# Optimization experiments

Measured on AMD Instinct MI355X. Metric: run time of the kernel, lower is better.

The kernel has to match this reference:

```python
import jax, jax.numpy as jnp
import numpy as np

F = 1024      # features
CF = 768      # context_features
H = 8         # num_heads
D = 64        # head_features
MID = H * D   # 512
SCALE = D ** -0.5


def _ln(x, g, b):
    m = jnp.mean(x, axis=-1, keepdims=True)
    v = jnp.var(x, axis=-1, keepdims=True)
    return (x - m) / jnp.sqrt(v + 1e-5) * g + b


def _attention(x, ctx, ng, nb, ncg, ncb, wq, wkv, wo, bo):
    # pre-norms (Attention.forward)
    xn = _ln(x, ng, nb)
    cn = _ln(ctx, ncg, ncb)
    q = xn @ wq                              # [b, n, MID]
    k, v = jnp.split(cn @ wkv, 2, axis=-1)   # [b, m, MID] each
    b, n, _ = q.shape
    m = k.shape[1]
    q = q.reshape(b, n, H, D).transpose(0, 2, 1, 3)  # b h n d
    k = k.reshape(b, m, H, D).transpose(0, 2, 1, 3)
    v = v.reshape(b, m, H, D).transpose(0, 2, 1, 3)
    sim = jnp.einsum('bhnd,bhmd->bhnm', q, k) * SCALE   # use_rel_pos=False
    attn = jax.nn.softmax(sim, axis=-1)
    out = jnp.einsum('bhnm,bhmd->bhnd', attn, v)
    out = out.transpose(0, 2, 1, 3).reshape(b, n, MID)
    return out @ wo + bo


def setup_inputs() -> dict:
    key = jax.random.key(0)
    ks = jax.random.split(key, 16)
    s = 0.02
    inp = {
        'x': jax.random.normal(ks[0], (4, 2048, F), jnp.float32),
        'context': jax.random.normal(ks[1], (4, 512, CF), jnp.float32),
        # self-attention params
        'sa_ng': jnp.ones((F,), jnp.float32),
        'sa_nb': jnp.zeros((F,), jnp.float32),
        'sa_ncg': jnp.ones((F,), jnp.float32),
        'sa_ncb': jnp.zeros((F,), jnp.float32),
        'sa_wq': jax.random.normal(ks[2], (F, MID), jnp.float32) * s,
        'sa_wkv': jax.random.normal(ks[3], (F, 2 * MID), jnp.float32) * s,
        'sa_wo': jax.random.normal(ks[4], (MID, F), jnp.float32) * s,
        'sa_bo': jnp.zeros((F,), jnp.float32),
        # cross-attention params
        'ca_ng': jnp.ones((F,), jnp.float32),
        'ca_nb': jnp.zeros((F,), jnp.float32),
        'ca_ncg': jnp.ones((CF,), jnp.float32),
        'ca_ncb': jnp.zeros((CF,), jnp.float32),
        'ca_wq': jax.random.normal(ks[5], (F, MID), jnp.float32) * s,
        'ca_wkv': jax.random.normal(ks[6], (CF, 2 * MID), jnp.float32) * s,
        'ca_wo': jax.random.normal(ks[7], (MID, F), jnp.float32) * s,
        'ca_bo': jnp.zeros((F,), jnp.float32),
    }
    return inp


def reference(x, context,
              sa_ng, sa_nb, sa_ncg, sa_ncb, sa_wq, sa_wkv, sa_wo, sa_bo,
              ca_ng, ca_nb, ca_ncg, ca_ncb, ca_wq, ca_wkv, ca_wo, ca_bo):
    # AttentionBlock.forward: x = self_attn(x) + x; x = cross_attn(x, ctx) + x
    x = _attention(x, x, sa_ng, sa_nb, sa_ncg, sa_ncb, sa_wq, sa_wkv, sa_wo, sa_bo) + x
    x = _attention(x, context, ca_ng, ca_nb, ca_ncg, ca_ncb, ca_wq, ca_wkv, ca_wo, ca_bo) + x
    return x
```

## Files before the change

### kernel.cpp

```cpp
#include <hip/hip_runtime.h>
#include <hip/hip_bf16.h>

typedef __bf16 bf16x8 __attribute__((ext_vector_type(8)));
typedef float  f32x4  __attribute__((ext_vector_type(4)));

#define MFMA16(a, b, c) __builtin_amdgcn_mfma_f32_16x16x32_bf16((a), (b), (c), 0, 0, 0)

__device__ __forceinline__ float fast_exp2(float x) {
#if __has_builtin(__builtin_amdgcn_exp2f)
    return __builtin_amdgcn_exp2f(x);
#else
    return exp2f(x);
#endif
}

__device__ __forceinline__ void async16(void* lds, const void* g) {
    __builtin_amdgcn_global_load_lds(
        (const __attribute__((address_space(1))) unsigned int*)g,
        (__attribute__((address_space(3))) unsigned int*)lds, 16, 0, 0);
}

__device__ __forceinline__ unsigned cvt_pk_bf16(float lo, float hi) {
    unsigned r;
    asm("v_cvt_pk_bf16_f32 %0, %1, %2" : "=v"(r) : "v"(lo), "v"(hi));
    return r;
}
__device__ __forceinline__ void pl32(unsigned& a, unsigned& b) {
    asm volatile("v_permlane32_swap_b32 %0, %1" : "+v"(a), "+v"(b));
}
__device__ __forceinline__ void pl16(unsigned& a, unsigned& b) {
    asm volatile("v_permlane16_swap_b32 %0, %1" : "+v"(a), "+v"(b));
}

__device__ __forceinline__ void tconv_tile(const float* __restrict__ W,
                                           __bf16* __restrict__ WT,
                                           int K, int N, int id, int nbx,
                                           __bf16 (*t)[65]) {
    int n0 = (id % nbx) * 64, k0 = (id / nbx) * 64;
    int tx = threadIdx.x & 63, ty = threadIdx.x >> 6;
#pragma unroll
    for (int r = ty; r < 64; r += 4)
        t[r][tx] = (__bf16)W[(size_t)(k0 + r) * N + n0 + tx];
    __syncthreads();
#pragma unroll
    for (int rr = ty; rr < 64; rr += 4)
        WT[(size_t)(n0 + rr) * K + k0 + tx] = t[tx][rr];
}

__global__ __launch_bounds__(256) void tconv6_kernel(
    const float* W0, __bf16* T0, const float* W1, __bf16* T1,
    const float* W2, __bf16* T2, const float* W3, __bf16* T3,
    const float* W4, __bf16* T4, const float* W5, __bf16* T5) {
    __shared__ __bf16 t[64][65];
    int id = blockIdx.x;
    if (id < 128)      tconv_tile(W0, T0, 1024, 512,  id,       8,  t);
    else if (id < 384) tconv_tile(W1, T1, 1024, 1024, id - 128, 16, t);
    else if (id < 512) tconv_tile(W2, T2, 512,  1024, id - 384, 16, t);
    else if (id < 640) tconv_tile(W3, T3, 1024, 512,  id - 512, 8,  t);
    else if (id < 832) tconv_tile(W4, T4, 768,  1024, id - 640, 16, t);
    else               tconv_tile(W5, T5, 512,  1024, id - 832, 16, t);
}

template <int C>
__device__ __forceinline__ void ln_body(const float* __restrict__ xr,
                                        const float* __restrict__ g,
                                        const float* __restrict__ b,
                                        __bf16* __restrict__ orow,
                                        float* p1, float* p2) {
    constexpr int NP = (C == 1024) ? 4 : 3;
    float v[NP], s1 = 0.f, s2 = 0.f;
    if constexpr (C == 1024) {
        float4 f = *(const float4*)&xr[threadIdx.x * 4];
        v[0] = f.x; v[1] = f.y; v[2] = f.z; v[3] = f.w;
#pragma unroll
        for (int i = 0; i < 4; i++) { s1 += v[i]; s2 += v[i] * v[i]; }
    } else {
#pragma unroll
        for (int i = 0; i < 3; i++) {
            v[i] = xr[threadIdx.x + i * 256];
            s1 += v[i]; s2 += v[i] * v[i];
        }
    }
#pragma unroll
    for (int off = 1; off < 64; off <<= 1) {
        s1 += __shfl_xor(s1, off);
        s2 += __shfl_xor(s2, off);
    }
    int wave = threadIdx.x >> 6;
    if ((threadIdx.x & 63) == 0) { p1[wave] = s1; p2[wave] = s2; }
    __syncthreads();
    s1 = p1[0] + p1[1] + p1[2] + p1[3];
    s2 = p2[0] + p2[1] + p2[2] + p2[3];
    float mean = s1 / C;
    float rstd = rsqrtf(s2 / C - mean * mean + 1e-5f);
    if constexpr (C == 1024) {
        union { __bf16 h[4]; unsigned long long u; } pk;
#pragma unroll
        for (int i = 0; i < 4; i++) {
            int c = threadIdx.x * 4 + i;
            pk.h[i] = (__bf16)((v[i] - mean) * rstd * g[c] + b[c]);
        }
        *(unsigned long long*)&orow[threadIdx.x * 4] = pk.u;
    } else {
#pragma unroll
        for (int i = 0; i < 3; i++) {
            int c = threadIdx.x + i * 256;
            orow[c] = (__bf16)((v[i] - mean) * rstd * g[c] + b[c]);
        }
    }
}

__global__ __launch_bounds__(256) void ln2_kernel(const float* __restrict__ x,
                                                  const float* __restrict__ g1,
                                                  const float* __restrict__ b1,
                                                  const float* __restrict__ g2,
                                                  const float* __restrict__ b2,
                                                  __bf16* __restrict__ o1,
                                                  __bf16* __restrict__ o2) {
    constexpr int C = 1024;
    int row = blockIdx.x;
    const float* xr = x + (size_t)row * C;
    float4 f = *(const float4*)&xr[threadIdx.x * 4];
    float v[4] = {f.x, f.y, f.z, f.w};
    float s1 = 0.f, s2 = 0.f;
#pragma unroll
    for (int i = 0; i < 4; i++) { s1 += v[i]; s2 += v[i] * v[i]; }
#pragma unroll
    for (int off = 1; off < 64; off <<= 1) {
        s1 += __shfl_xor(s1, off);
        s2 += __shfl_xor(s2, off);
    }
    __shared__ float p1[4], p2[4];
    int wave = threadIdx.x >> 6;
    if ((threadIdx.x & 63) == 0) { p1[wave] = s1; p2[wave] = s2; }
    __syncthreads();
    s1 = p1[0] + p1[1] + p1[2] + p1[3];
    s2 = p2[0] + p2[1] + p2[2] + p2[3];
    float mean = s1 / C;
    float rstd = rsqrtf(s2 / C - mean * mean + 1e-5f);
    union { __bf16 h[4]; unsigned long long u; } pk1, pk2;
#pragma unroll
    for (int i = 0; i < 4; i++) {
        int c = threadIdx.x * 4 + i;
        float nv = (v[i] - mean) * rstd;
        pk1.h[i] = (__bf16)(nv * g1[c] + b1[c]);
        pk2.h[i] = (__bf16)(nv * g2[c] + b2[c]);
    }
    *(unsigned long long*)&o1[(size_t)row * C + threadIdx.x * 4] = pk1.u;
    *(unsigned long long*)&o2[(size_t)row * C + threadIdx.x * 4] = pk2.u;
}

__global__ __launch_bounds__(256) void ln_cross_kernel(
    const float* __restrict__ x1, const float* __restrict__ g1, const float* __restrict__ b1,
    __bf16* __restrict__ o1,
    const float* __restrict__ ctx, const float* __restrict__ g2, const float* __restrict__ b2,
    __bf16* __restrict__ o2, int rows1) {
    __shared__ float p1[4], p2[4];
    int id = blockIdx.x;
    if (id < rows1) {
        ln_body<1024>(x1 + (size_t)id * 1024, g1, b1, o1 + (size_t)id * 1024, p1, p2);
    } else {
        int row = id - rows1;
        ln_body<768>(ctx + (size_t)row * 768, g2, b2, o2 + (size_t)row * 768, p1, p2);
    }
}

template <int EPI>
__device__ __forceinline__ void gemm_core(const __bf16* __restrict__ A,
                                          const __bf16* __restrict__ BT,
                                          void* __restrict__ Cout,
                                          int N, int K, int bm, int bn,
                                          const float* __restrict__ bias,
                                          const float* __restrict__ res,
                                          float scale,
                                          __bf16* Al, __bf16* Bl) {
    int tid = threadIdx.x;
    int lane = tid & 63, wave = tid >> 6;
    int quad = lane >> 4, l15 = lane & 15;
    int wm = wave >> 1, wn = wave & 1;
    const __bf16* Ab = A + (size_t)(bm * 128) * K;
    const __bf16* Bb = BT + (size_t)(bn * 128) * K;
    f32x4 acc[4][4] = {};
    for (int k0 = 0; k0 < K; k0 += 64) {
#pragma unroll
        for (int j = 0; j < 4; j++) {
            int sbase = wave * 256 + j * 64;
            int s = sbase + lane;
            int r = s >> 3, c = (s & 7) ^ (r & 7);
            async16((char*)Al + sbase * 16, &Ab[(size_t)r * K + k0 + c * 8]);
            async16((char*)Bl + sbase * 16, &Bb[(size_t)r * K + k0 + c * 8]);
        }
        __syncthreads();
#pragma unroll
        for (int ks = 0; ks < 2; ks++) {
            bf16x8 a[4], b[4];
#pragma unroll
            for (int i = 0; i < 4; i++) {
                int row = wm * 64 + i * 16 + l15;
                a[i] = *(const bf16x8*)&Al[row * 64 + ((ks * 4 + quad) ^ (row & 7)) * 8];
            }
#pragma unroll
            for (int t = 0; t < 4; t++) {
                int row = wn * 64 + t * 16 + l15;
                b[t] = *(const bf16x8*)&Bl[row * 64 + ((ks * 4 + quad) ^ (row & 7)) * 8];
            }
#pragma unroll
            for (int i = 0; i < 4; i++)
#pragma unroll
                for (int t = 0; t < 4; t++) acc[i][t] = MFMA16(a[i], b[t], acc[i][t]);
        }
        __syncthreads();
    }
#pragma unroll
    for (int i = 0; i < 4; i++) {
#pragma unroll
        for (int t = 0; t < 4; t++) {
#pragma unroll
            for (int r = 0; r < 4; r++) {
                int row = bm * 128 + wm * 64 + i * 16 + quad * 4 + r;
                int col = bn * 128 + wn * 64 + t * 16 + l15;
                float vv = acc[i][t][r];
                if (EPI == 0) {
                    ((__bf16*)Cout)[(size_t)row * N + col] = (__bf16)(vv * scale);
                } else {
                    ((float*)Cout)[(size_t)row * N + col] =
                        vv + bias[col] + res[(size_t)row * N + col];
                }
            }
        }
    }
}

template <int EPI>
__global__ __launch_bounds__(256) void gemm_bt(const __bf16* __restrict__ A,
                                               const __bf16* __restrict__ BT,
                                               void* __restrict__ Cout,
                                               int M, int N, int K,
                                               const float* __restrict__ bias,
                                               const float* __restrict__ res) {
    __shared__ __align__(16) __bf16 Al[128 * 64];
    __shared__ __align__(16) __bf16 Bl[128 * 64];
    gemm_core<EPI>(A, BT, Cout, N, K, blockIdx.x, blockIdx.y, bias, res, 1.0f, Al, Bl);
}

__global__ __launch_bounds__(256) void gemm_fused3(
    const __bf16* A0, const __bf16* B0, __bf16* C0, int N0, int K0, int nbn0, float sc0,
    const __bf16* A1, const __bf16* B1, __bf16* C1, int N1, int K1, int nbn1, float sc1,
    const __bf16* A2, const __bf16* B2, __bf16* C2, int N2, int K2, int nbn2, float sc2,
    int c0, int c1) {
    __shared__ __align__(16) __bf16 Al[128 * 64];
    __shared__ __align__(16) __bf16 Bl[128 * 64];
    int id = blockIdx.x;
    if (id < c0) {
        gemm_core<0>(A0, B0, C0, N0, K0, id / nbn0, id % nbn0, nullptr, nullptr, sc0, Al, Bl);
    } else if (id < c1) {
        id -= c0;
        gemm_core<0>(A1, B1, C1, N1, K1, id / nbn1, id % nbn1, nullptr, nullptr, sc1, Al, Bl);
    } else {
        id -= c1;
        gemm_core<0>(A2, B2, C2, N2, K2, id / nbn2, id % nbn2, nullptr, nullptr, sc2, Al, Bl);
    }
}

__global__ __launch_bounds__(256) void flash_kernel(const __bf16* __restrict__ q,
                                                    const __bf16* __restrict__ kb,
                                                    const __bf16* __restrict__ vt,
                                                    __bf16* __restrict__ out,
                                                    int n, int m) {
    __shared__ __align__(16) __bf16 Ks[2][2][64 * 64];
    __shared__ __align__(16) __bf16 VTs[2][2][64 * 64];
    int tid = threadIdx.x;
    int lane = tid & 63, w = tid >> 6;
    int quad = lane >> 4, l15 = lane & 15;
    int qt = blockIdx.x, h = blockIdx.y, b = blockIdx.z;
    const size_t BM = (size_t)gridDim.z * m;

    const __bf16* qbase = q + (size_t)(b * n + qt * 128 + w * 32) * 512 + h * 64;
    bf16x8 qf[2][2];
#pragma unroll
    for (int s = 0; s < 2; s++)
#pragma unroll
        for (int u = 0; u < 2; u++)
            qf[s][u] = *(const bf16x8*)&qbase[(u * 16 + l15) * 512 + s * 32 + quad * 8];

    int s0 = w * 128 + lane, s1 = s0 + 64;
    int r0 = s0 >> 3, c0 = (s0 & 7) ^ (r0 & 7);
    int r1 = s1 >> 3, c1 = (s1 & 7) ^ (r1 & 7);
    const int sb0 = (w * 128) * 16, sb1 = sb0 + 64 * 16;
    const __bf16* ksrc0 = &kb[(size_t)(b * m + r0) * 512 + h * 64 + (size_t)c0 * 8];
    const __bf16* ksrc1 = &kb[(size_t)(b * m + r1) * 512 + h * 64 + (size_t)c1 * 8];
    const __bf16* vsrc0 = &vt[(size_t)(h * 64 + r0) * BM + b * m + (size_t)c0 * 8];
    const __bf16* vsrc1 = &vt[(size_t)(h * 64 + r1) * BM + b * m + (size_t)c1 * 8];
    const size_t kadv = (size_t)64 * 512;
    const int vadv = 64;

    f32x4 acc[2][4] = {};
    float lp[2] = {0.f, 0.f};
    int npair = m / 128;

#pragma unroll
    for (int tt = 0; tt < 2; tt++) {
        async16((char*)Ks[0][tt] + sb0, ksrc0);
        async16((char*)Ks[0][tt] + sb1, ksrc1);
        async16((char*)VTs[0][tt] + sb0, vsrc0);
        async16((char*)VTs[0][tt] + sb1, vsrc1);
        ksrc0 += kadv; ksrc1 += kadv; vsrc0 += vadv; vsrc1 += vadv;
    }

    for (int j = 0; j < npair; j++) {
        int pb = j & 1;
        __syncthreads();
        if (j + 1 < npair) {
#pragma unroll
            for (int tt = 0; tt < 2; tt++) {
                async16((char*)Ks[pb ^ 1][tt] + sb0, ksrc0);
                async16((char*)Ks[pb ^ 1][tt] + sb1, ksrc1);
                async16((char*)VTs[pb ^ 1][tt] + sb0, vsrc0);
                async16((char*)VTs[pb ^ 1][tt] + sb1, vsrc1);
                ksrc0 += kadv; ksrc1 += kadv; vsrc0 += vadv; vsrc1 += vadv;
            }
        }

#pragma unroll
        for (int tt = 0; tt < 2; tt++) {
            const __bf16* Kc = Ks[pb][tt];
            const __bf16* Vc = VTs[pb][tt];

            unsigned pkl[4][2], pkh[4][2];
#pragma unroll
            for (int t = 0; t < 4; t++) {
                int krow = t * 16 + l15;
                bf16x8 ak0 = *(const bf16x8*)&Kc[krow * 64 + ((quad) ^ (krow & 7)) * 8];
                bf16x8 ak1 = *(const bf16x8*)&Kc[krow * 64 + ((4 + quad) ^ (krow & 7)) * 8];
                f32x4 sc[2] = {};
#pragma unroll
                for (int u = 0; u < 2; u++) {
                    sc[u] = MFMA16(ak0, qf[0][u], sc[u]);
                    sc[u] = MFMA16(ak1, qf[1][u], sc[u]);
                }
#pragma unroll
                for (int u = 0; u < 2; u++) {
                    float e0 = fast_exp2(sc[u][0]);
                    float e1 = fast_exp2(sc[u][1]);
                    float e2 = fast_exp2(sc[u][2]);
                    float e3 = fast_exp2(sc[u][3]);
                    lp[u] += (e0 + e1) + (e2 + e3);
                    pkl[t][u] = cvt_pk_bf16(e0, e1);
                    pkh[t][u] = cvt_pk_bf16(e2, e3);
                }
            }

            bf16x8 ap[2][2];
#pragma unroll
            for (int s = 0; s < 2; s++)
#pragma unroll
                for (int u = 0; u < 2; u++) {
                    unsigned a = pkl[2 * s][u], c = pkl[2 * s + 1][u];
                    pl32(a, c); pl16(a, c);
                    unsigned bb = pkh[2 * s][u], d = pkh[2 * s + 1][u];
                    pl32(bb, d); pl16(bb, d);
                    union { unsigned wd[4]; bf16x8 v; } pu;
                    pu.wd[0] = a; pu.wd[1] = bb; pu.wd[2] = c; pu.wd[3] = d;
                    ap[s][u] = pu.v;
                }

#pragma unroll
            for (int s = 0; s < 2; s++)
#pragma unroll
                for (int t2 = 0; t2 < 4; t2++) {
                    int drow = t2 * 16 + l15;
                    int jv = (s * 4 + quad) ^ (drow & 7);
                    bf16x8 bv = *(const bf16x8*)&Vc[drow * 64 + jv * 8];
#pragma unroll
                    for (int u = 0; u < 2; u++)
                        acc[u][t2] = MFMA16(ap[s][u], bv, acc[u][t2]);
                }
        }
    }

#pragma unroll
    for (int u = 0; u < 2; u++) {
        lp[u] += __shfl_xor(lp[u], 16);
        lp[u] += __shfl_xor(lp[u], 32);
    }
    float rinv0 = 1.0f / lp[0];
    float rinv1 = 1.0f / lp[1];
#pragma unroll
    for (int u = 0; u < 2; u++) {
#pragma unroll
        for (int r = 0; r < 4; r++) {
            float rl = __shfl(u == 0 ? rinv0 : rinv1, quad * 4 + r);
            int row = b * n + qt * 128 + w * 32 + u * 16 + quad * 4 + r;
#pragma unroll
            for (int t2 = 0; t2 < 4; t2++)
                out[(size_t)row * 512 + h * 64 + t2 * 16 + l15] =
                    (__bf16)(acc[u][t2][r] * rl);
        }
    }
}

extern "C" void kernel_launch(void* const* d_in, const int* in_sizes, int n_in,
                              void* d_out, int out_size, void* d_ws, size_t ws_size,
                              hipStream_t stream) {
    const float* x      = (const float*)d_in[0];
    const float* ctx    = (const float*)d_in[1];
    const float* sa_ng  = (const float*)d_in[2];
    const float* sa_nb  = (const float*)d_in[3];
    const float* sa_ncg = (const float*)d_in[4];
    const float* sa_ncb = (const float*)d_in[5];
    const float* sa_wq  = (const float*)d_in[6];
    const float* sa_wkv = (const float*)d_in[7];
    const float* sa_wo  = (const float*)d_in[8];
    const float* sa_bo  = (const float*)d_in[9];
    const float* ca_ng  = (const float*)d_in[10];
    const float* ca_nb  = (const float*)d_in[11];
    const float* ca_ncg = (const float*)d_in[12];
    const float* ca_ncb = (const float*)d_in[13];
    const float* ca_wq  = (const float*)d_in[14];
    const float* ca_wkv = (const float*)d_in[15];
    const float* ca_wo  = (const float*)d_in[16];
    const float* ca_bo  = (const float*)d_in[17];
    float* out = (float*)d_out;

    const int B = 4, N = 2048, M = 512, F = 1024, CF = 768, MID = 512;
    const int ROWS = B * N;
    const int CROWS = B * M;
    const float QSCALE = 0.125f * 1.4426950408889634f;

    char* ws = (char*)d_ws;
    size_t off = 0;
    auto alloc = [&](size_t bytes) {
        void* p = ws + off;
        off = (off + bytes + 255) & ~(size_t)255;
        return p;
    };
    __bf16* wqT   = (__bf16*)alloc((size_t)MID * F * 2);
    __bf16* wkvT  = (__bf16*)alloc((size_t)(2 * MID) * F * 2);
    __bf16* woT   = (__bf16*)alloc((size_t)F * MID * 2);
    __bf16* cwqT  = (__bf16*)alloc((size_t)MID * F * 2);
    __bf16* cwkvT = (__bf16*)alloc((size_t)(2 * MID) * CF * 2);
    __bf16* cwoT  = (__bf16*)alloc((size_t)F * MID * 2);
    __bf16* xn1   = (__bf16*)alloc((size_t)ROWS * F * 2);
    __bf16* xn2   = (__bf16*)alloc((size_t)ROWS * F * 2);
    __bf16* qb    = (__bf16*)alloc((size_t)ROWS * MID * 2);
    __bf16* kb    = (__bf16*)alloc((size_t)ROWS * MID * 2);
    __bf16* vt    = (__bf16*)alloc((size_t)MID * ROWS * 2);
    __bf16* ao    = (__bf16*)alloc((size_t)ROWS * MID * 2);
    float*  x1    = (float*)alloc((size_t)ROWS * F * 4);
    (void)ws_size; (void)in_sizes; (void)n_in; (void)out_size;

    dim3 blk(256);

    tconv6_kernel<<<dim3(960), blk, 0, stream>>>(
        sa_wq, wqT, sa_wkv, wkvT, sa_wo, woT, ca_wq, cwqT, ca_wkv, cwkvT, ca_wo, cwoT);

    ln2_kernel<<<dim3(ROWS), blk, 0, stream>>>(x, sa_ng, sa_nb, sa_ncg, sa_ncb, xn1, xn2);
    {
        int c0 = (ROWS / 128) * (MID / 128);
        int c1 = c0 + (ROWS / 128) * (MID / 128);
        int c2 = c1 + (MID / 128) * (ROWS / 128);
        gemm_fused3<<<dim3(c2), blk, 0, stream>>>(
            xn1, wqT, qb, MID, F, MID / 128, QSCALE,
            xn2, wkvT, kb, MID, F, MID / 128, 1.0f,
            wkvT + (size_t)MID * F, xn2, vt, ROWS, F, ROWS / 128, 1.0f,
            c0, c1);
    }
    flash_kernel<<<dim3(N / 128, 8, B), blk, 0, stream>>>(qb, kb, vt, ao, N, N);
    gemm_bt<1><<<dim3(ROWS / 128, F / 128), blk, 0, stream>>>(
        ao, woT, x1, ROWS, F, MID, sa_bo, x);

    ln_cross_kernel<<<dim3(ROWS + CROWS), blk, 0, stream>>>(
        x1, ca_ng, ca_nb, xn1, ctx, ca_ncg, ca_ncb, xn2, ROWS);
    {
        int c0 = (ROWS / 128) * (MID / 128);
        int c1 = c0 + (CROWS / 128) * (MID / 128);
        int c2 = c1 + (MID / 128) * (CROWS / 128);
        gemm_fused3<<<dim3(c2), blk, 0, stream>>>(
            xn1, cwqT, qb, MID, F, MID / 128, QSCALE,
            xn2, cwkvT, kb, MID, CF, MID / 128, 1.0f,
            cwkvT + (size_t)MID * CF, xn2, vt, CROWS, CF, CROWS / 128, 1.0f,
            c0, c1);
    }
    flash_kernel<<<dim3(N / 128, 8, B), blk, 0, stream>>>(qb, kb, vt, ao, N, M);
    gemm_bt<1><<<dim3(ROWS / 128, F / 128), blk, 0, stream>>>(
        ao, cwoT, out, ROWS, F, MID, ca_bo, x1);
}
```

Before: 306.2 us.

## Split flash attention KV range across two wave groups with LDS reduction

The flash kernel now launches 512 threads per block, with two groups of four waves each processing half of the key/value sequence for the same 128 query rows. Partial accumulators and row sums from the second half are combined with the first through LDS before normalisation and the store. This doubles the waves available per query tile to hide latency and raise occupancy. In exchange it adds a reduction through shared memory and extra synchronisation, and it uses single 64-row tiles instead of pairs per iteration.

```diff
diff --git a/kernel.cpp b/kernel.cpp
--- a/kernel.cpp
+++ b/kernel.cpp
@@ -262,20 +262,22 @@
     }
 }
 
-__global__ __launch_bounds__(256) void flash_kernel(const __bf16* __restrict__ q,
-                                                    const __bf16* __restrict__ kb,
-                                                    const __bf16* __restrict__ vt,
-                                                    __bf16* __restrict__ out,
-                                                    int n, int m) {
-    __shared__ __align__(16) __bf16 Ks[2][2][64 * 64];
-    __shared__ __align__(16) __bf16 VTs[2][2][64 * 64];
+__global__ __launch_bounds__(512, 4) void flash_kernel(const __bf16* __restrict__ q,
+                                                       const __bf16* __restrict__ kb,
+                                                       const __bf16* __restrict__ vt,
+                                                       __bf16* __restrict__ out,
+                                                       int n, int m) {
+    __shared__ __align__(16) __bf16 stage[2][2][2][64 * 64];
+    __shared__ float Lbuf[4][32];
     int tid = threadIdx.x;
     int lane = tid & 63, w = tid >> 6;
+    int half = w >> 2, wl = w & 3;
     int quad = lane >> 4, l15 = lane & 15;
     int qt = blockIdx.x, h = blockIdx.y, b = blockIdx.z;
     const size_t BM = (size_t)gridDim.z * m;
-
-    const __bf16* qbase = q + (size_t)(b * n + qt * 128 + w * 32) * 512 + h * 64;
+    const int mh = m >> 1;
+
+    const __bf16* qbase = q + (size_t)(b * n + qt * 128 + wl * 32) * 512 + h * 64;
     bf16x8 qf[2][2];
 #pragma unroll
     for (int s = 0; s < 2; s++)
@@ -283,99 +285,90 @@
         for (int u = 0; u < 2; u++)
             qf[s][u] = *(const bf16x8*)&qbase[(u * 16 + l15) * 512 + s * 32 + quad * 8];
 
-    int s0 = w * 128 + lane, s1 = s0 + 64;
+    int s0 = wl * 128 + lane, s1 = s0 + 64;
     int r0 = s0 >> 3, c0 = (s0 & 7) ^ (r0 & 7);
     int r1 = s1 >> 3, c1 = (s1 & 7) ^ (r1 & 7);
-    const int sb0 = (w * 128) * 16, sb1 = sb0 + 64 * 16;
-    const __bf16* ksrc0 = &kb[(size_t)(b * m + r0) * 512 + h * 64 + (size_t)c0 * 8];
-    const __bf16* ksrc1 = &kb[(size_t)(b * m + r1) * 512 + h * 64 + (size_t)c1 * 8];
-    const __bf16* vsrc0 = &vt[(size_t)(h * 64 + r0) * BM + b * m + (size_t)c0 * 8];
-    const __bf16* vsrc1 = &vt[(size_t)(h * 64 + r1) * BM + b * m + (size_t)c1 * 8];
+    const int sb0 = (wl * 128) * 16, sb1 = sb0 + 64 * 16;
+    const __bf16* ksrc0 = &kb[(size_t)(b * m + half * mh + r0) * 512 + h * 64 + (size_t)c0 * 8];
+    const __bf16* ksrc1 = &kb[(size_t)(b * m + half * mh + r1) * 512 + h * 64 + (size_t)c1 * 8];
+    const __bf16* vsrc0 = &vt[(size_t)(h * 64 + r0) * BM + b * m + half * mh + (size_t)c0 * 8];
+    const __bf16* vsrc1 = &vt[(size_t)(h * 64 + r1) * BM + b * m + half * mh + (size_t)c1 * 8];
     const size_t kadv = (size_t)64 * 512;
     const int vadv = 64;
 
+    __bf16* Kst[2] = {&stage[0][half][0][0], &stage[0][half][1][0]};
+    __bf16* Vst[2] = {&stage[1][half][0][0], &stage[1][half][1][0]};
+
     f32x4 acc[2][4] = {};
     float lp[2] = {0.f, 0.f};
-    int npair = m / 128;
-
-#pragma unroll
-    for (int tt = 0; tt < 2; tt++) {
-        async16((char*)Ks[0][tt] + sb0, ksrc0);
-        async16((char*)Ks[0][tt] + sb1, ksrc1);
-        async16((char*)VTs[0][tt] + sb0, vsrc0);
-        async16((char*)VTs[0][tt] + sb1, vsrc1);
-        ksrc0 += kadv; ksrc1 += kadv; vsrc0 += vadv; vsrc1 += vadv;
-    }
-
-    for (int j = 0; j < npair; j++) {
-        int pb = j & 1;
+    int nkt = mh / 64;
+
+    async16((char*)Kst[0] + sb0, ksrc0);
+    async16((char*)Kst[0] + sb1, ksrc1);
+    async16((char*)Vst[0] + sb0, vsrc0);
+    async16((char*)Vst[0] + sb1, vsrc1);
+
+    for (int kt = 0; kt < nkt; kt++) {
+        const __bf16* Kc = Kst[kt & 1];
+        const __bf16* Vc = Vst[kt & 1];
         __syncthreads();
-        if (j + 1 < npair) {
-#pragma unroll
-            for (int tt = 0; tt < 2; tt++) {
-                async16((char*)Ks[pb ^ 1][tt] + sb0, ksrc0);
-                async16((char*)Ks[pb ^ 1][tt] + sb1, ksrc1);
-                async16((char*)VTs[pb ^ 1][tt] + sb0, vsrc0);
-                async16((char*)VTs[pb ^ 1][tt] + sb1, vsrc1);
-                ksrc0 += kadv; ksrc1 += kadv; vsrc0 += vadv; vsrc1 += vadv;
-            }
-        }
-
-#pragma unroll
-        for (int tt = 0; tt < 2; tt++) {
-            const __bf16* Kc = Ks[pb][tt];
-            const __bf16* Vc = VTs[pb][tt];
-
-            unsigned pkl[4][2], pkh[4][2];
-#pragma unroll
-            for (int t = 0; t < 4; t++) {
-                int krow = t * 16 + l15;
-                bf16x8 ak0 = *(const bf16x8*)&Kc[krow * 64 + ((quad) ^ (krow & 7)) * 8];
-                bf16x8 ak1 = *(const bf16x8*)&Kc[krow * 64 + ((4 + quad) ^ (krow & 7)) * 8];
-                f32x4 sc[2] = {};
-#pragma unroll
-                for (int u = 0; u < 2; u++) {
-                    sc[u] = MFMA16(ak0, qf[0][u], sc[u]);
-                    sc[u] = MFMA16(ak1, qf[1][u], sc[u]);
-                }
-#pragma unroll
-                for (int u = 0; u < 2; u++) {
-                    float e0 = fast_exp2(sc[u][0]);
-                    float e1 = fast_exp2(sc[u][1]);
-                    float e2 = fast_exp2(sc[u][2]);
-                    float e3 = fast_exp2(sc[u][3]);
-                    lp[u] += (e0 + e1) + (e2 + e3);
-                    pkl[t][u] = cvt_pk_bf16(e0, e1);
-                    pkh[t][u] = cvt_pk_bf16(e2, e3);
-                }
-            }
-
-            bf16x8 ap[2][2];
-#pragma unroll
-            for (int s = 0; s < 2; s++)
-#pragma unroll
-                for (int u = 0; u < 2; u++) {
-                    unsigned a = pkl[2 * s][u], c = pkl[2 * s + 1][u];
-                    pl32(a, c); pl16(a, c);
-                    unsigned bb = pkh[2 * s][u], d = pkh[2 * s + 1][u];
-                    pl32(bb, d); pl16(bb, d);
-                    union { unsigned wd[4]; bf16x8 v; } pu;
-                    pu.wd[0] = a; pu.wd[1] = bb; pu.wd[2] = c; pu.wd[3] = d;
-                    ap[s][u] = pu.v;
-                }
-
-#pragma unroll
-            for (int s = 0; s < 2; s++)
-#pragma unroll
-                for (int t2 = 0; t2 < 4; t2++) {
-                    int drow = t2 * 16 + l15;
-                    int jv = (s * 4 + quad) ^ (drow & 7);
-                    bf16x8 bv = *(const bf16x8*)&Vc[drow * 64 + jv * 8];
-#pragma unroll
-                    for (int u = 0; u < 2; u++)
-                        acc[u][t2] = MFMA16(ap[s][u], bv, acc[u][t2]);
-                }
-        }
+        if (kt + 1 < nkt) {
+            ksrc0 += kadv; ksrc1 += kadv; vsrc0 += vadv; vsrc1 += vadv;
+            async16((char*)Kst[(kt + 1) & 1] + sb0, ksrc0);
+            async16((char*)Kst[(kt + 1) & 1] + sb1, ksrc1);
+            async16((char*)Vst[(kt + 1) & 1] + sb0, vsrc0);
+            async16((char*)Vst[(kt + 1) & 1] + sb1, vsrc1);
+        }
+
+        unsigned pkl[4][2], pkh[4][2];
+#pragma unroll
+        for (int t = 0; t < 4; t++) {
+            int krow = t * 16 + l15;
+            bf16x8 ak0 = *(const bf16x8*)&Kc[krow * 64 + ((quad) ^ (krow & 7)) * 8];
+            bf16x8 ak1 = *(const bf16x8*)&Kc[krow * 64 + ((4 + quad) ^ (krow & 7)) * 8];
+            f32x4 sc[2] = {};
+#pragma unroll
+            for (int u = 0; u < 2; u++) {
+                sc[u] = MFMA16(ak0, qf[0][u], sc[u]);
+                sc[u] = MFMA16(ak1, qf[1][u], sc[u]);
+            }
+#pragma unroll
+            for (int u = 0; u < 2; u++) {
+                float e0 = fast_exp2(sc[u][0]);
+                float e1 = fast_exp2(sc[u][1]);
+                float e2 = fast_exp2(sc[u][2]);
+                float e3 = fast_exp2(sc[u][3]);
+                lp[u] += (e0 + e1) + (e2 + e3);
+                pkl[t][u] = cvt_pk_bf16(e0, e1);
+                pkh[t][u] = cvt_pk_bf16(e2, e3);
+            }
+        }
+
+        bf16x8 ap[2][2];
+#pragma unroll
+        for (int s = 0; s < 2; s++)
+#pragma unroll
+            for (int u = 0; u < 2; u++) {
+                unsigned a = pkl[2 * s][u], c = pkl[2 * s + 1][u];
+                pl32(a, c); pl16(a, c);
+                unsigned bb = pkh[2 * s][u], d = pkh[2 * s + 1][u];
+                pl32(bb, d); pl16(bb, d);
+                union { unsigned wd[4]; bf16x8 v; } pu;
+                pu.wd[0] = a; pu.wd[1] = bb; pu.wd[2] = c; pu.wd[3] = d;
+                ap[s][u] = pu.v;
+            }
+
+#pragma unroll
+        for (int s = 0; s < 2; s++)
+#pragma unroll
+            for (int t2 = 0; t2 < 4; t2++) {
+                int drow = t2 * 16 + l15;
+                int jv = (s * 4 + quad) ^ (drow & 7);
+                bf16x8 bv = *(const bf16x8*)&Vc[drow * 64 + jv * 8];
+#pragma unroll
+                for (int u = 0; u < 2; u++)
+                    acc[u][t2] = MFMA16(ap[s][u], bv, acc[u][t2]);
+            }
     }
 
 #pragma unroll
@@ -383,18 +376,46 @@
         lp[u] += __shfl_xor(lp[u], 16);
         lp[u] += __shfl_xor(lp[u], 32);
     }
-    float rinv0 = 1.0f / lp[0];
-    float rinv1 = 1.0f / lp[1];
-#pragma unroll
-    for (int u = 0; u < 2; u++) {
-#pragma unroll
-        for (int r = 0; r < 4; r++) {
-            float rl = __shfl(u == 0 ? rinv0 : rinv1, quad * 4 + r);
-            int row = b * n + qt * 128 + w * 32 + u * 16 + quad * 4 + r;
+
+    __syncthreads();
+    float* Fbuf = (float*)&stage[0][0][0][0];
+    if (half == 1) {
+#pragma unroll
+        for (int u = 0; u < 2; u++) {
 #pragma unroll
             for (int t2 = 0; t2 < 4; t2++)
-                out[(size_t)row * 512 + h * 64 + t2 * 16 + l15] =
-                    (__bf16)(acc[u][t2][r] * rl);
+#pragma unroll
+                for (int r = 0; r < 4; r++)
+                    Fbuf[wl * 2080 + (u * 16 + quad * 4 + r) * 65 + t2 * 16 + l15] =
+                        acc[u][t2][r];
+            if (quad == 0) Lbuf[wl][u * 16 + l15] = lp[u];
+        }
+    }
+    __syncthreads();
+    if (half == 0) {
+#pragma unroll
+        for (int u = 0; u < 2; u++) {
+            lp[u] += Lbuf[wl][u * 16 + l15];
+#pragma unroll
+            for (int t2 = 0; t2 < 4; t2++)
+#pragma unroll
+                for (int r = 0; r < 4; r++)
+                    acc[u][t2][r] +=
+                        Fbuf[wl * 2080 + (u * 16 + quad * 4 + r) * 65 + t2 * 16 + l15];
+        }
+        float rinv0 = 1.0f / lp[0];
+        float rinv1 = 1.0f / lp[1];
+#pragma unroll
+        for (int u = 0; u < 2; u++) {
+#pragma unroll
+            for (int r = 0; r < 4; r++) {
+                float rl = __shfl(u == 0 ? rinv0 : rinv1, quad * 4 + r);
+                int row = b * n + qt * 128 + wl * 32 + u * 16 + quad * 4 + r;
+#pragma unroll
+                for (int t2 = 0; t2 < 4; t2++)
+                    out[(size_t)row * 512 + h * 64 + t2 * 16 + l15] =
+                        (__bf16)(acc[u][t2][r] * rl);
+            }
         }
     }
 }
@@ -450,6 +471,7 @@
     (void)ws_size; (void)in_sizes; (void)n_in; (void)out_size;
 
     dim3 blk(256);
+    dim3 fblk(512);
 
     tconv6_kernel<<<dim3(960), blk, 0, stream>>>(
         sa_wq, wqT, sa_wkv, wkvT, sa_wo, woT, ca_wq, cwqT, ca_wkv, cwkvT, ca_wo, cwoT);
@@ -465,7 +487,7 @@
             wkvT + (size_t)MID * F, xn2, vt, ROWS, F, ROWS / 128, 1.0f,
             c0, c1);
     }
-    flash_kernel<<<dim3(N / 128, 8, B), blk, 0, stream>>>(qb, kb, vt, ao, N, N);
+    flash_kernel<<<dim3(N / 128, 8, B), fblk, 0, stream>>>(qb, kb, vt, ao, N, N);
     gemm_bt<1><<<dim3(ROWS / 128, F / 128), blk, 0, stream>>>(
         ao, woT, x1, ROWS, F, MID, sa_bo, x);
 
@@ -481,7 +503,7 @@
             cwkvT + (size_t)MID * CF, xn2, vt, CROWS, CF, CROWS / 128, 1.0f,
             c0, c1);
     }
-    flash_kernel<<<dim3(N / 128, 8, B), blk, 0, stream>>>(qb, kb, vt, ao, N, M);
+    flash_kernel<<<dim3(N / 128, 8, B), fblk, 0, stream>>>(qb, kb, vt, ao, N, M);
     gemm_bt<1><<<dim3(ROWS / 128, F / 128), blk, 0, stream>>>(
         ao, cwoT, out, ROWS, F, MID, ca_bo, x1);
 }
```

Result: slower. 348.2 us (+13.7%).
